# Kernel tuning notes

Hardware: AMD Instinct MI355X
Metric: run time of the kernel (lower is better)

## Reference

```python
import jax, jax.numpy as jnp
import numpy as np

N = 100000
E = 1600000
D_PCA = 50
D_BIO = 64
HID = 32
HEADS = 4
OUT = 50
EPS = 1e-5


def setup_inputs() -> dict:
    key = jax.random.key(0)
    ks = jax.random.split(key, 32)
    g = lambda i, shape, s=0.05: jax.random.normal(ks[i], shape, dtype=jnp.float32) * s
    inp = {
        'x_pca': jax.random.normal(ks[0], (N, D_PCA), dtype=jnp.float32),
        'x_bio': jax.random.normal(ks[1], (N, D_BIO), dtype=jnp.float32),
        'edge_index': jax.random.randint(ks[2], (2, E), 0, N, dtype=jnp.int32),
        # bio encoder: Linear(64,16) -> BN(16) -> ELU -> Linear(16,16) -> ELU
        'bioW1': g(3, (16, D_BIO)), 'biob1': g(4, (16,)),
        'bn0_g': 1.0 + g(5, (16,)), 'bn0_b': g(6, (16,)),
        'bn0_m': g(7, (16,)), 'bn0_v': 1.0 + 0.1 * jax.random.uniform(ks[8], (16,), dtype=jnp.float32),
        'bioW2': g(9, (16, 16)), 'biob2': g(10, (16,)),
        # GATv2 layer 1: in = 50+16 = 66, out = HEADS*HID concat
        'Wl1': g(11, (HEADS * HID, D_PCA + 16)), 'bl1': g(12, (HEADS * HID,)),
        'Wr1': g(13, (HEADS * HID, D_PCA + 16)), 'br1': g(14, (HEADS * HID,)),
        'att1': g(15, (HEADS, HID)), 'bias1': g(16, (HEADS * HID,)),
        'bn1_g': 1.0 + g(17, (HEADS * HID,)), 'bn1_b': g(18, (HEADS * HID,)),
        'bn1_m': g(19, (HEADS * HID,)), 'bn1_v': 1.0 + 0.1 * jax.random.uniform(ks[20], (HEADS * HID,), dtype=jnp.float32),
        # GATv2 layer 2: in = HEADS*HID, heads=1, concat=False
        'Wl2': g(21, (HID, HEADS * HID)), 'bl2': g(22, (HID,)),
        'Wr2': g(23, (HID, HEADS * HID)), 'br2': g(24, (HID,)),
        'att2': g(25, (1, HID)), 'bias2': g(26, (HID,)),
        'bn2_g': 1.0 + g(27, (HID,)), 'bn2_b': g(28, (HID,)),
        'bn2_m': g(29, (HID,)), 'bn2_v': 1.0 + 0.1 * jax.random.uniform(ks[30], (HID,), dtype=jnp.float32),
        'predW': g(31, (OUT, HID)), 'predb': jnp.zeros((OUT,), dtype=jnp.float32),
    }
    return inp


def _bn(h, gm, bt, mean, var):
    # BatchNorm1d in eval mode (running stats)
    return (h - mean) * jax.lax.rsqrt(var + EPS) * gm + bt


def _gatv2(x, src, dst, Wl, bl, Wr, br, att, bias, heads, out_dim, concat):
    n = x.shape[0]
    xl = (x @ Wl.T + bl).reshape(n, heads, out_dim)  # source transform
    xr = (x @ Wr.T + br).reshape(n, heads, out_dim)  # target transform
    e = jax.nn.leaky_relu(xl[src] + xr[dst], 0.2)    # [E,H,C]
    logits = jnp.einsum('ehc,hc->eh', e, att)        # [E,H]
    m = jax.ops.segment_max(logits, dst, num_segments=n)
    a = jnp.exp(logits - m[dst])
    denom = jax.ops.segment_sum(a, dst, num_segments=n)
    alpha = a / (denom[dst] + 1e-16)                 # segment softmax over dst
    out = jax.ops.segment_sum(xl[src] * alpha[..., None], dst, num_segments=n)
    out = out.reshape(n, heads * out_dim) if concat else out.mean(axis=1)
    return out + bias


def reference(x_pca, x_bio, edge_index,
              bioW1, biob1, bn0_g, bn0_b, bn0_m, bn0_v, bioW2, biob2,
              Wl1, bl1, Wr1, br1, att1, bias1, bn1_g, bn1_b, bn1_m, bn1_v,
              Wl2, bl2, Wr2, br2, att2, bias2, bn2_g, bn2_b, bn2_m, bn2_v,
              predW, predb):
    n = x_pca.shape[0]
    # add self-loops (PyG GATv2Conv default)
    loop = jnp.arange(n, dtype=edge_index.dtype)
    src = jnp.concatenate([edge_index[0], loop])
    dst = jnp.concatenate([edge_index[1], loop])

    # bio encoder
    h_bio = jax.nn.elu(_bn(x_bio @ bioW1.T + biob1, bn0_g, bn0_b, bn0_m, bn0_v))
    h_bio = jax.nn.elu(h_bio @ bioW2.T + biob2)
    x = jnp.concatenate([x_pca, h_bio], axis=1)  # [N, 66]

    h = _gatv2(x, src, dst, Wl1, bl1, Wr1, br1, att1, bias1, HEADS, HID, True)
    h = jax.nn.elu(_bn(h, bn1_g, bn1_b, bn1_m, bn1_v))  # dropout off (eval)
    h = _gatv2(h, src, dst, Wl2, bl2, Wr2, br2, att2, bias2, 1, HID, False)
    h = jax.nn.elu(_bn(h, bn2_g, bn2_b, bn2_m, bn2_v))
    return h @ predW.T + predb
```

## Files before the change

kernel.cpp:

```cpp
#include <hip/hip_runtime.h>
#include <hip/hip_fp16.h>
#include <cstdint>
#include <cstddef>

#define NN 100000
#define NE 1600000
#define NEP (NE + NN)
#define NBLK 200
#define CHUNK ((NEP + NBLK - 1) / NBLK)
#define NBUCK2 ((NN + 255) / 256)
#define HISTN (NBUCK2 * NBLK)
#define HSCAN_BLOCKS ((HISTN + 1023) / 1024)

typedef __attribute__((ext_vector_type(8))) _Float16 half8;
typedef __attribute__((ext_vector_type(4))) _Float16 h4v;
typedef __attribute__((ext_vector_type(2))) _Float16 h2v;
typedef __attribute__((ext_vector_type(4))) float float4v;

__device__ __forceinline__ float elu_f(float x) {
    return x > 0.f ? x : __expf(x) - 1.f;
}

__device__ __forceinline__ float ex2(float x) {
#if __has_builtin(__builtin_amdgcn_exp2f)
    return __builtin_amdgcn_exp2f(x);
#else
    return exp2f(x);
#endif
}

template<int CTRL>
__device__ __forceinline__ float dpp_add(float x) {
    int s = __builtin_amdgcn_update_dpp(0, __float_as_int(x), CTRL, 0xF, 0xF, true);
    return x + __int_as_float(s);
}
__device__ __forceinline__ float sum4_all(float x) {
    x = dpp_add<0xB1>(x); x = dpp_add<0x4E>(x);
    return x;
}
__device__ __forceinline__ float sum8_all(float x) {
    x = dpp_add<0xB1>(x); x = dpp_add<0x4E>(x); x = dpp_add<0x141>(x);
    return x;
}

__device__ __forceinline__ float dot2f(h2v a, h2v b, float c) {
#if __has_builtin(__builtin_amdgcn_fdot2)
    return __builtin_amdgcn_fdot2(a, b, c, false);
#else
    return fmaf((float)a[0], (float)b[0], fmaf((float)a[1], (float)b[1], c));
#endif
}

__device__ __forceinline__ h2v hmax2v(h2v a, h2v b) {
#if __has_builtin(__builtin_elementwise_max)
    return __builtin_elementwise_max(a, b);
#else
    __half2 r = __hmax2(*(__half2*)&a, *(__half2*)&b);
    return *(h2v*)&r;
#endif
}


__global__ __launch_bounds__(256) void part_hist(const int* __restrict__ ei, int* __restrict__ hist)
{
    __shared__ int cnt[NBUCK2];
    int tid = threadIdx.x, k = blockIdx.x;
    for (int i = tid; i < NBUCK2; i += 256) cnt[i] = 0;
    __syncthreads();
    int e0 = k * CHUNK, e1 = min(e0 + CHUNK, NEP);
    for (int e = e0 + tid; e < e1; e += 256) {
        int dst = (e < NE) ? ei[NE + e] : e - NE;
        atomicAdd(&cnt[dst >> 8], 1);
    }
    __syncthreads();
    for (int i = tid; i < NBUCK2; i += 256) hist[i * NBLK + k] = cnt[i];
}

__global__ __launch_bounds__(256) void scan_p1(const int* __restrict__ src, int* __restrict__ part, int n)
{
    __shared__ int wsum[4];
    int t = threadIdx.x;
    int i0 = blockIdx.x * 1024 + t * 4;
    int s = 0;
    if (i0 + 3 < n) { int4 d = *(const int4*)(src + i0); s = d.x + d.y + d.z + d.w; }
    else { for (int k = 0; k < 4; k++) if (i0 + k < n) s += src[i0 + k]; }
    for (int d = 1; d < 64; d <<= 1) s += __shfl_xor(s, d, 64);
    if ((t & 63) == 0) wsum[t >> 6] = s;
    __syncthreads();
    if (t == 0) part[blockIdx.x] = wsum[0] + wsum[1] + wsum[2] + wsum[3];
}

__global__ __launch_bounds__(128) void scan_p2(int* __restrict__ part, int nb, int* __restrict__ off)
{
    __shared__ int wt[2];
    int t = threadIdx.x;
    int lane = t & 63, w = t >> 6;
    int v = (t < nb) ? part[t] : 0;
    int x = v;
    for (int d = 1; d < 64; d <<= 1) { int y = __shfl_up(x, d, 64); if (lane >= d) x += y; }
    if (lane == 63) wt[w] = x;
    __syncthreads();
    int base = (w == 1) ? wt[0] : 0;
    int excl = base + x - v;
    if (t < nb) part[t] = excl;
    if (t == 0) off[NN] = NEP;
}

__global__ __launch_bounds__(256) void scan_p3(int* __restrict__ data, const int* __restrict__ part, int n)
{
    __shared__ int wsum[4];
    int t = threadIdx.x, lane = t & 63, w = t >> 6;
    int i0 = blockIdx.x * 1024 + t * 4;
    int d0 = 0, d1 = 0, d2 = 0, d3 = 0;
    if (i0 + 3 < n) { int4 d = *(const int4*)(data + i0); d0 = d.x; d1 = d.y; d2 = d.z; d3 = d.w; }
    else if (i0 < n) {
        d0 = data[i0];
        if (i0 + 1 < n) d1 = data[i0 + 1];
        if (i0 + 2 < n) d2 = data[i0 + 2];
    }
    int s = d0 + d1 + d2 + d3;
    int x = s;
    for (int d = 1; d < 64; d <<= 1) { int y = __shfl_up(x, d, 64); if (lane >= d) x += y; }
    if (lane == 63) wsum[w] = x;
    __syncthreads();
    int wb = 0;
    for (int i = 0; i < w; i++) wb += wsum[i];
    int base = part[blockIdx.x] + wb + x - s;
    if (i0 < n)     data[i0]     = base;
    if (i0 + 1 < n) data[i0 + 1] = base + d0;
    if (i0 + 2 < n) data[i0 + 2] = base + d0 + d1;
    if (i0 + 3 < n) data[i0 + 3] = base + d0 + d1 + d2;
}

__global__ __launch_bounds__(256) void part_scatter(const int* __restrict__ ei,
                                                    const int* __restrict__ hist,
                                                    unsigned* __restrict__ ebuf)
{
    __shared__ int cur[NBUCK2];
    int tid = threadIdx.x, k = blockIdx.x;
    for (int i = tid; i < NBUCK2; i += 256) cur[i] = hist[i * NBLK + k];
    __syncthreads();
    int e0 = k * CHUNK, e1 = min(e0 + CHUNK, NEP);
    for (int e = e0 + tid; e < e1; e += 256) {
        int src, dst;
        if (e < NE) { src = ei[e]; dst = ei[NE + e]; } else { src = dst = e - NE; }
        int pos = atomicAdd(&cur[dst >> 8], 1);
        ebuf[pos] = (unsigned)src | ((unsigned)(dst & 255) << 24);
    }
}

__global__ __launch_bounds__(256) void bucket_csr(const int* __restrict__ hist,
                                                  const unsigned* __restrict__ ebuf,
                                                  int* __restrict__ off, int* __restrict__ csr)
{
    __shared__ int cnt[256];
    __shared__ int cur[256];
    __shared__ int wsum[4];
    int b = blockIdx.x;
    int d0 = b << 8;
    int tid = threadIdx.x;
    int e0 = hist[b * NBLK];
    int e1 = (b + 1 < NBUCK2) ? hist[(b + 1) * NBLK] : NEP;
    cnt[tid] = 0;
    __syncthreads();
    for (int i = e0 + tid; i < e1; i += 256) atomicAdd(&cnt[ebuf[i] >> 24], 1);
    __syncthreads();
    int c = cnt[tid];
    int x = c;
    int lane = tid & 63, w = tid >> 6;
    for (int d = 1; d < 64; d <<= 1) { int y = __shfl_up(x, d, 64); if (lane >= d) x += y; }
    if (lane == 63) wsum[w] = x;
    __syncthreads();
    int wb = 0;
    for (int i = 0; i < w; i++) wb += wsum[i];
    int excl = wb + x - c;
    cur[tid] = e0 + excl;
    int node = d0 + tid;
    if (node < NN) off[node] = e0 + excl;
    __syncthreads();
    for (int i = e0 + tid; i < e1; i += 256) {
        unsigned v = ebuf[i];
        int p = atomicAdd(&cur[v >> 24], 1);
        csr[p] = (int)(v & 0xFFFFFF);
    }
}


__global__ __launch_bounds__(256) void bio_kernel(
    const float* __restrict__ xb, const float* __restrict__ xp,
    const float* __restrict__ W1, const float* __restrict__ b1,
    const float* __restrict__ g0, const float* __restrict__ bb0,
    const float* __restrict__ m0, const float* __restrict__ v0,
    const float* __restrict__ W2, const float* __restrict__ b2,
    __half* __restrict__ xh)
{
    __shared__ float sW1[16*64], sW2[16*16], sb1[16], sb2[16], ss[16], st[16];
    int tid = threadIdx.x;
    for (int idx = tid; idx < 1024; idx += 256) sW1[idx] = W1[idx];
    if (tid < 256) sW2[tid] = W2[tid];
    if (tid < 16) {
        sb1[tid] = b1[tid]; sb2[tid] = b2[tid];
        float s = g0[tid] * rsqrtf(v0[tid] + 1e-5f);
        ss[tid] = s; st[tid] = bb0[tid] - m0[tid] * s;
    }
    __syncthreads();
    int i = blockIdx.x * 256 + tid;
    if (i >= NN) return;
    float bio[64];
    const float4* p = (const float4*)(xb + (size_t)i * 64);
    #pragma unroll
    for (int q = 0; q < 16; q++) {
        float4 f = p[q];
        bio[q*4] = f.x; bio[q*4+1] = f.y; bio[q*4+2] = f.z; bio[q*4+3] = f.w;
    }
    float t1[16];
    #pragma unroll
    for (int j = 0; j < 16; j++) {
        float acc = sb1[j];
        #pragma unroll
        for (int k = 0; k < 64; k++) acc += bio[k] * sW1[j*64 + k];
        acc = acc * ss[j] + st[j];
        t1[j] = elu_f(acc);
    }
    __half* xrow = xh + (size_t)i * 96;
    const float* xpr = xp + (size_t)i * 50;
    #pragma unroll
    for (int j = 0; j < 25; j++) {
        float2 f = *(const float2*)(xpr + 2 * j);
        *(__half2*)(xrow + 2 * j) = __floats2half2_rn(f.x, f.y);
    }
    #pragma unroll
    for (int j = 0; j < 16; j++) {
        float acc = sb2[j];
        #pragma unroll
        for (int k = 0; k < 16; k++) acc += t1[k] * sW2[j*16 + k];
        xrow[50 + j] = __float2half(elu_f(acc));
    }
    __half2 z2 = __floats2half2_rn(0.f, 0.f);
    #pragma unroll
    for (int j = 0; j < 15; j++) *(__half2*)(xrow + 66 + 2 * j) = z2;
}


__global__ __launch_bounds__(256) void wconvert_all(
    const float* __restrict__ Wl1, const float* __restrict__ Wr1,
    const float* __restrict__ bl1, const float* __restrict__ br1,
    const float* __restrict__ Wl2, const float* __restrict__ Wr2,
    const float* __restrict__ bl2, const float* __restrict__ br2,
    const float* __restrict__ predW, const float* __restrict__ predb,
    const float* __restrict__ bias1, const float* __restrict__ bn1g,
    const float* __restrict__ bn1b, const float* __restrict__ bn1m,
    const float* __restrict__ bn1v,
    const float* __restrict__ bias2, const float* __restrict__ bn2g,
    const float* __restrict__ bn2b, const float* __restrict__ bn2m,
    const float* __restrict__ bn2v,
    __half* __restrict__ wcat1, float* __restrict__ bcat1,
    __half* __restrict__ wcat2, float* __restrict__ bcat2,
    __half* __restrict__ wpred, float* __restrict__ bpred,
    float* __restrict__ scb1, float* __restrict__ shb1,
    float* __restrict__ scb2, float* __restrict__ shb2)
{
    int t = blockIdx.x * 256 + threadIdx.x;
    if (t < 256 * 96) {
        int j = t / 96, k = t - j * 96;
        float v = (k < 66) ? ((j < 128) ? Wl1[j * 66 + k] : Wr1[(j - 128) * 66 + k]) : 0.f;
        wcat1[t] = __float2half(v);
    }
    int u = t - 256 * 96;
    if (u >= 0 && u < 64 * 128) {
        int j = u >> 7, k = u & 127;
        float v = (j < 32) ? Wl2[j * 128 + k] : Wr2[(j - 32) * 128 + k];
        wcat2[u] = __float2half(v);
    }
    int w = u - 64 * 128;
    if (w >= 0 && w < 64 * 32) {
        int j = w >> 5;
        wpred[w] = __float2half(j < 50 ? predW[w] : 0.f);
    }
    int z = w - 64 * 32;
    if (z >= 0 && z < 256) bcat1[z] = (z < 128) ? bl1[z] : br1[z - 128];
    int z2 = z - 256;
    if (z2 >= 0 && z2 < 64) bcat2[z2] = (z2 < 32) ? bl2[z2] : br2[z2 - 32];
    int z3 = z2 - 64;
    if (z3 >= 0 && z3 < 64) bpred[z3] = (z3 < 50) ? predb[z3] : 0.f;
    int z4 = z3 - 64;
    if (z4 >= 0 && z4 < 128) {
        float sc = bn1g[z4] * rsqrtf(bn1v[z4] + 1e-5f);
        scb1[z4] = sc;
        shb1[z4] = bn1b[z4] + (bias1[z4] - bn1m[z4]) * sc;
    }
    int z5 = z4 - 128;
    if (z5 >= 0 && z5 < 32) {
        float sc = bn2g[z5] * rsqrtf(bn2v[z5] + 1e-5f);
        scb2[z5] = sc;
        shb2[z5] = bn2b[z5] + (bias2[z5] - bn2m[z5]) * sc;
    }
}

template<int KT, int NC, bool FOUT>
__global__ __launch_bounds__(256) void mfma_gemm(
    const __half* __restrict__ in, const __half* __restrict__ wcat,
    const float* __restrict__ bcat, void* __restrict__ outv, int n, int ncol)
{
    constexpr int K = KT * 32;
    constexpr int KP = K + 8;
    __shared__ __half sW[NC * KP];
    __shared__ __half sX[64 * KP];
    __shared__ float sB[NC];
    int tid = threadIdx.x;
    for (int idx = tid * 8; idx < NC * K; idx += 256 * 8) {
        int r = idx / K, c = idx - r * K;
        *(half8*)(&sW[r * KP + c]) = *(const half8*)(&wcat[r * K + c]);
    }
    for (int idx = tid; idx < NC; idx += 256) sB[idx] = bcat[idx];
    int row0 = blockIdx.x * 64;
    half8 hz = {0, 0, 0, 0, 0, 0, 0, 0};
    for (int idx = tid * 8; idx < 64 * K; idx += 256 * 8) {
        int r = idx / K, c = idx - r * K;
        int gr = row0 + r;
        half8 v = (gr < n) ? *(const half8*)(&in[(size_t)gr * K + c]) : hz;
        *(half8*)(&sX[r * KP + c]) = v;
    }
    __syncthreads();
    int w = tid >> 6, lane = tid & 63;
    int m = lane & 15, quad = lane >> 4;
    half8 a[KT];
    #pragma unroll
    for (int kt = 0; kt < KT; kt++)
        a[kt] = *(const half8*)(&sX[(w * 16 + m) * KP + kt * 32 + quad * 8]);
    #pragma unroll 1
    for (int nt = 0; nt < NC / 16; nt++) {
        float4v acc = {0.f, 0.f, 0.f, 0.f};
        #pragma unroll
        for (int kt = 0; kt < KT; kt++) {
            half8 bfrag = *(const half8*)(&sW[(nt * 16 + m) * KP + kt * 32 + quad * 8]);
            acc = __builtin_amdgcn_mfma_f32_16x16x32_f16(a[kt], bfrag, acc, 0, 0, 0);
        }
        int col = nt * 16 + m;
        float bias = sB[col];
        #pragma unroll
        for (int i = 0; i < 4; i++) {
            int r = row0 + w * 16 + quad * 4 + i;
            if (r < n) {
                if (FOUT) { if (col < ncol) ((float*)outv)[(size_t)r * ncol + col] = acc[i] + bias; }
                else ((__half*)outv)[(size_t)r * NC + col] = __float2half(acc[i] + bias);
            }
        }
    }
}

__global__ __launch_bounds__(256) void fused_gat1(
    const int* __restrict__ off, const int* __restrict__ csr,
    const __half* __restrict__ xcat, const float* __restrict__ att,
    const float* __restrict__ scb, const float* __restrict__ shb,
    __half* __restrict__ h1)
{
    int wave = threadIdx.x >> 6;
    int lane = threadIdx.x & 63;
    int node = blockIdx.x * 4 + wave;
    if (node >= NN) return;
    int row = lane >> 4;
    int cl  = lane & 15;
    int ch  = cl * 8;
    unsigned chb = (unsigned)cl * 16u;
    const char* xbase = (const char*)xcat;
    const float LOG2E = 1.44269504088896f;

    half8 xr8 = *(const half8*)(xbase + (size_t)node * 512 + 256 + chb);
    float4 af0 = *(const float4*)(att + ch);
    float4 af1 = *(const float4*)(att + ch + 4);
    h2v a01 = {(_Float16)(af0.x * LOG2E), (_Float16)(af0.y * LOG2E)};
    h2v a23 = {(_Float16)(af0.z * LOG2E), (_Float16)(af0.w * LOG2E)};
    h2v a45 = {(_Float16)(af1.x * LOG2E), (_Float16)(af1.y * LOG2E)};
    h2v a67 = {(_Float16)(af1.z * LOG2E), (_Float16)(af1.w * LOG2E)};
    h2v xr01 = {xr8[0], xr8[1]}, xr23 = {xr8[2], xr8[3]};
    h2v xr45 = {xr8[4], xr8[5]}, xr67 = {xr8[6], xr8[7]};
    const h2v c2 = {(_Float16)0.2f, (_Float16)0.2f};

    int k0 = off[node], k1 = off[node + 1];
    float acc0 = 0.f, acc1 = 0.f, acc2 = 0.f, acc3 = 0.f;
    float acc4 = 0.f, acc5 = 0.f, acc6 = 0.f, acc7 = 0.f, denom = 0.f;

    int rowp4 = row + 4;

    auto edge = [&](half8 cur, bool valid) {
        h2v xl01 = {cur[0], cur[1]}, xl23 = {cur[2], cur[3]};
        h2v xl45 = {cur[4], cur[5]}, xl67 = {cur[6], cur[7]};
        h2v s01 = xl01 + xr01, s23 = xl23 + xr23;
        h2v s45 = xl45 + xr45, s67 = xl67 + xr67;
        h2v l01 = hmax2v(s01, s01 * c2);
        h2v l23 = hmax2v(s23, s23 * c2);
        h2v l45 = hmax2v(s45, s45 * c2);
        h2v l67 = hmax2v(s67, s67 * c2);
        float pp = dot2f(l01, a01, dot2f(l23, a23, dot2f(l45, a45, dot2f(l67, a67, 0.f))));
        pp = sum4_all(pp);
        float wgt = valid ? ex2(pp) : 0.f;
        denom += wgt;
        acc0 = fmaf((float)cur[0], wgt, acc0);
        acc1 = fmaf((float)cur[1], wgt, acc1);
        acc2 = fmaf((float)cur[2], wgt, acc2);
        acc3 = fmaf((float)cur[3], wgt, acc3);
        acc4 = fmaf((float)cur[4], wgt, acc4);
        acc5 = fmaf((float)cur[5], wgt, acc5);
        acc6 = fmaf((float)cur[6], wgt, acc6);
        acc7 = fmaf((float)cur[7], wgt, acc7);
    };

    for (int base = k0; base < k1; base += 64) {
        int nb = min(64, k1 - base);
        int mysrc = (lane < nb) ? csr[base + lane] : 0;
        int pairs = (nb + 7) >> 3;

        auto loadpair = [&](half8& A, half8& B, int j) {
            int i0 = __shfl(mysrc, j * 8 + row, 64);
            int i1 = __shfl(mysrc, j * 8 + rowp4, 64);
            A = *(const half8*)(xbase + (((unsigned)i0 << 9) + chb));
            B = *(const half8*)(xbase + (((unsigned)i1 << 9) + chb));
        };
        auto edgepair = [&](half8 A, half8 B, int j) {
            edge(A, (j * 8 + row) < nb);
            edge(B, (j * 8 + rowp4) < nb);
        };

        half8 A0, B0, A1, B1, A2, B2;
        loadpair(A0, B0, 0);
        if (pairs > 1) loadpair(A1, B1, 1);
        if (pairs > 2) loadpair(A2, B2, 2);
        int j = 0;
        while (true) {
            edgepair(A0, B0, j); if (j + 3 < pairs) loadpair(A0, B0, j + 3); if (++j >= pairs) break;
            edgepair(A1, B1, j); if (j + 3 < pairs) loadpair(A1, B1, j + 3); if (++j >= pairs) break;
            edgepair(A2, B2, j); if (j + 3 < pairs) loadpair(A2, B2, j + 3); if (++j >= pairs) break;
        }
    }
    acc0 += __shfl_xor(acc0, 16, 64); acc0 += __shfl_xor(acc0, 32, 64);
    acc1 += __shfl_xor(acc1, 16, 64); acc1 += __shfl_xor(acc1, 32, 64);
    acc2 += __shfl_xor(acc2, 16, 64); acc2 += __shfl_xor(acc2, 32, 64);
    acc3 += __shfl_xor(acc3, 16, 64); acc3 += __shfl_xor(acc3, 32, 64);
    acc4 += __shfl_xor(acc4, 16, 64); acc4 += __shfl_xor(acc4, 32, 64);
    acc5 += __shfl_xor(acc5, 16, 64); acc5 += __shfl_xor(acc5, 32, 64);
    acc6 += __shfl_xor(acc6, 16, 64); acc6 += __shfl_xor(acc6, 32, 64);
    acc7 += __shfl_xor(acc7, 16, 64); acc7 += __shfl_xor(acc7, 32, 64);
    denom += __shfl_xor(denom, 16, 64); denom += __shfl_xor(denom, 32, 64);
    if (row == 0) {
        float inv = 1.f / (denom + 1e-16f);
        float4 s0 = *(const float4*)(scb + ch), s1 = *(const float4*)(scb + ch + 4);
        float4 h0 = *(const float4*)(shb + ch), h1f = *(const float4*)(shb + ch + 4);
        float o[8];
        o[0] = elu_f(fmaf(acc0 * inv, s0.x, h0.x));
        o[1] = elu_f(fmaf(acc1 * inv, s0.y, h0.y));
        o[2] = elu_f(fmaf(acc2 * inv, s0.z, h0.z));
        o[3] = elu_f(fmaf(acc3 * inv, s0.w, h0.w));
        o[4] = elu_f(fmaf(acc4 * inv, s1.x, h1f.x));
        o[5] = elu_f(fmaf(acc5 * inv, s1.y, h1f.y));
        o[6] = elu_f(fmaf(acc6 * inv, s1.z, h1f.z));
        o[7] = elu_f(fmaf(acc7 * inv, s1.w, h1f.w));
        half8 oh = {(_Float16)o[0], (_Float16)o[1], (_Float16)o[2], (_Float16)o[3],
                    (_Float16)o[4], (_Float16)o[5], (_Float16)o[6], (_Float16)o[7]};
        *(half8*)(h1 + (size_t)node * 128 + ch) = oh;
    }
}

__global__ __launch_bounds__(256) void fused_gat2(
    const int* __restrict__ off, const int* __restrict__ csr,
    const __half* __restrict__ xcat2, const float* __restrict__ att,
    const float* __restrict__ scb, const float* __restrict__ shb,
    __half* __restrict__ h2)
{
    int wave = threadIdx.x >> 6;
    int lane = threadIdx.x & 63;
    int node = blockIdx.x * 4 + wave;
    if (node >= NN) return;
    int row = lane >> 3;
    int cl  = lane & 7;
    int ch  = cl * 4;
    unsigned chb = (unsigned)cl * 8u;
    const char* xbase = (const char*)xcat2;
    const float LOG2E = 1.44269504088896f;

    h4v xr4 = *(const h4v*)(xbase + (size_t)node * 128 + 64 + chb);
    h2v xr01 = {xr4[0], xr4[1]}, xr23 = {xr4[2], xr4[3]};
    float4 af = *(const float4*)(att + ch);
    h2v a01 = {(_Float16)(af.x * LOG2E), (_Float16)(af.y * LOG2E)};
    h2v a23 = {(_Float16)(af.z * LOG2E), (_Float16)(af.w * LOG2E)};
    const h2v c2 = {(_Float16)0.2f, (_Float16)0.2f};

    int k0 = off[node], k1 = off[node + 1];
    float acc0 = 0.f, acc1 = 0.f, acc2 = 0.f, acc3 = 0.f, denom = 0.f;

    int rowp8 = row + 8;

    auto edge = [&](h4v cur, bool valid) {
        h2v xl01 = {cur[0], cur[1]}, xl23 = {cur[2], cur[3]};
        h2v s01 = xl01 + xr01, s23 = xl23 + xr23;
        h2v l01 = hmax2v(s01, s01 * c2);
        h2v l23 = hmax2v(s23, s23 * c2);
        float pp = dot2f(l01, a01, dot2f(l23, a23, 0.f));
        pp = sum8_all(pp);
        float wgt = valid ? ex2(pp) : 0.f;
        denom += wgt;
        acc0 = fmaf((float)cur[0], wgt, acc0);
        acc1 = fmaf((float)cur[1], wgt, acc1);
        acc2 = fmaf((float)cur[2], wgt, acc2);
        acc3 = fmaf((float)cur[3], wgt, acc3);
    };

    for (int base = k0; base < k1; base += 64) {
        int nb = min(64, k1 - base);
        int mysrc = (lane < nb) ? csr[base + lane] : 0;
        int pairs = (nb + 15) >> 4;

        auto loadpair = [&](h4v& A, h4v& B, int j) {
            int i0 = __shfl(mysrc, j * 16 + row, 64);
            int i1 = __shfl(mysrc, j * 16 + rowp8, 64);
            A = *(const h4v*)(xbase + (((unsigned)i0 << 7) + chb));
            B = *(const h4v*)(xbase + (((unsigned)i1 << 7) + chb));
        };
        auto edgepair = [&](h4v A, h4v B, int j) {
            edge(A, (j * 16 + row) < nb);
            edge(B, (j * 16 + rowp8) < nb);
        };

        h4v A0, B0, A1, B1, A2, B2;
        loadpair(A0, B0, 0);
        if (pairs > 1) loadpair(A1, B1, 1);
        if (pairs > 2) loadpair(A2, B2, 2);
        int j = 0;
        while (true) {
            edgepair(A0, B0, j); if (j + 3 < pairs) loadpair(A0, B0, j + 3); if (++j >= pairs) break;
            edgepair(A1, B1, j); if (j + 3 < pairs) loadpair(A1, B1, j + 3); if (++j >= pairs) break;
            edgepair(A2, B2, j); if (j + 3 < pairs) loadpair(A2, B2, j + 3); if (++j >= pairs) break;
        }
    }
    acc0 += __shfl_xor(acc0, 8, 64); acc0 += __shfl_xor(acc0, 16, 64); acc0 += __shfl_xor(acc0, 32, 64);
    acc1 += __shfl_xor(acc1, 8, 64); acc1 += __shfl_xor(acc1, 16, 64); acc1 += __shfl_xor(acc1, 32, 64);
    acc2 += __shfl_xor(acc2, 8, 64); acc2 += __shfl_xor(acc2, 16, 64); acc2 += __shfl_xor(acc2, 32, 64);
    acc3 += __shfl_xor(acc3, 8, 64); acc3 += __shfl_xor(acc3, 16, 64); acc3 += __shfl_xor(acc3, 32, 64);
    denom += __shfl_xor(denom, 8, 64); denom += __shfl_xor(denom, 16, 64); denom += __shfl_xor(denom, 32, 64);
    if (row == 0) {
        float inv = 1.f / (denom + 1e-16f);
        float4 sv = *(const float4*)(scb + ch);
        float4 hv = *(const float4*)(shb + ch);
        float o0 = elu_f(fmaf(acc0 * inv, sv.x, hv.x));
        float o1 = elu_f(fmaf(acc1 * inv, sv.y, hv.y));
        float o2 = elu_f(fmaf(acc2 * inv, sv.z, hv.z));
        float o3 = elu_f(fmaf(acc3 * inv, sv.w, hv.w));
        h4v oh = {(_Float16)o0, (_Float16)o1, (_Float16)o2, (_Float16)o3};
        *(h4v*)(h2 + (size_t)node * 32 + ch) = oh;
    }
}

extern "C" void kernel_launch(void* const* d_in, const int* in_sizes, int n_in,
                              void* d_out, int out_size, void* d_ws, size_t ws_size,
                              hipStream_t stream)
{
    const float* x_pca = (const float*)d_in[0];
    const float* x_bio = (const float*)d_in[1];
    const int*   ei    = (const int*)d_in[2];
    const float* bioW1 = (const float*)d_in[3];
    const float* biob1 = (const float*)d_in[4];
    const float* bn0_g = (const float*)d_in[5];
    const float* bn0_b = (const float*)d_in[6];
    const float* bn0_m = (const float*)d_in[7];
    const float* bn0_v = (const float*)d_in[8];
    const float* bioW2 = (const float*)d_in[9];
    const float* biob2 = (const float*)d_in[10];
    const float* Wl1   = (const float*)d_in[11];
    const float* bl1   = (const float*)d_in[12];
    const float* Wr1   = (const float*)d_in[13];
    const float* br1   = (const float*)d_in[14];
    const float* att1  = (const float*)d_in[15];
    const float* bias1 = (const float*)d_in[16];
    const float* bn1_g = (const float*)d_in[17];
    const float* bn1_b = (const float*)d_in[18];
    const float* bn1_m = (const float*)d_in[19];
    const float* bn1_v = (const float*)d_in[20];
    const float* Wl2   = (const float*)d_in[21];
    const float* bl2   = (const float*)d_in[22];
    const float* Wr2   = (const float*)d_in[23];
    const float* br2   = (const float*)d_in[24];
    const float* att2  = (const float*)d_in[25];
    const float* bias2 = (const float*)d_in[26];
    const float* bn2_g = (const float*)d_in[27];
    const float* bn2_b = (const float*)d_in[28];
    const float* bn2_m = (const float*)d_in[29];
    const float* bn2_v = (const float*)d_in[30];
    const float* predW = (const float*)d_in[31];
    const float* predb = (const float*)d_in[32];

    float* ws = (float*)d_ws;
    __half* xh    = (__half*)ws;
    float*  p0    = ws + 4800000;
    __half* xcat1 = (__half*)p0;
    float*  p1    = p0 + 12800000;
    __half* h1h   = (__half*)p1;
    float*  p2    = p1 + 6400000;
    __half* xcat2 = (__half*)p2;
    float*  p3    = p2 + 3200000;
    __half* h2h   = (__half*)p3;
    float*  p4    = p3 + 1600000;
    __half* wcat1 = (__half*)p4;
    float*  bcat1 = p4 + 12288;
    __half* wcat2 = (__half*)(bcat1 + 256);
    float*  bcat2 = bcat1 + 256 + 4096;
    __half* wpred = (__half*)(bcat2 + 64);
    float*  bpred = bcat2 + 64 + 1024;
    float*  scb1  = bpred + 64;
    float*  shb1  = scb1 + 128;
    float*  scb2  = shb1 + 128;
    float*  shb2  = scb2 + 32;
    int*    ib    = (int*)(shb2 + 32);
    unsigned* ebuf = (unsigned*)ib;
    int*    hist   = ib + NEP;
    int*    part   = hist + HISTN;
    int*    off    = part + 128;
    int*    csr    = off + NN + 1;

    float* out = (float*)d_out;

    part_hist<<<NBLK, 256, 0, stream>>>(ei, hist);
    scan_p1<<<HSCAN_BLOCKS, 256, 0, stream>>>(hist, part, HISTN);
    scan_p2<<<1, 128, 0, stream>>>(part, HSCAN_BLOCKS, off);
    scan_p3<<<HSCAN_BLOCKS, 256, 0, stream>>>(hist, part, HISTN);
    part_scatter<<<NBLK, 256, 0, stream>>>(ei, hist, ebuf);
    bucket_csr<<<NBUCK2, 256, 0, stream>>>(hist, ebuf, off, csr);

    bio_kernel<<<(NN + 255) / 256, 256, 0, stream>>>(
        x_bio, x_pca, bioW1, biob1, bn0_g, bn0_b, bn0_m, bn0_v, bioW2, biob2, xh);

    wconvert_all<<<139, 256, 0, stream>>>(
        Wl1, Wr1, bl1, br1, Wl2, Wr2, bl2, br2, predW, predb,
        bias1, bn1_g, bn1_b, bn1_m, bn1_v,
        bias2, bn2_g, bn2_b, bn2_m, bn2_v,
        wcat1, bcat1, wcat2, bcat2, wpred, bpred,
        scb1, shb1, scb2, shb2);

    mfma_gemm<3, 256, false><<<(NN + 63) / 64, 256, 0, stream>>>(xh, wcat1, bcat1, xcat1, NN, 0);

    fused_gat1<<<(NN + 3) / 4, 256, 0, stream>>>(
        off, csr, xcat1, att1, scb1, shb1, h1h);

    mfma_gemm<4, 64, false><<<(NN + 63) / 64, 256, 0, stream>>>(h1h, wcat2, bcat2, xcat2, NN, 0);

    fused_gat2<<<(NN + 3) / 4, 256, 0, stream>>>(
        off, csr, xcat2, att2, scb2, shb2, h2h);

    mfma_gemm<1, 64, true><<<(NN + 63) / 64, 256, 0, stream>>>(h2h, wpred, bpred, out, NN, 50);
}
```

Measured before the change: 413.2 us.

## Split GATv2 source/target projections into separate arrays and simplify gather prefetch

The GEMM now writes the source (xl) and target (xr) projections to two separate contiguous arrays instead of one interleaved row. The gather in both GAT kernels then reads from a denser xl table with half the row stride, which is meant to improve cache and TLB locality for the random source-node gathers. The triple-buffered prefetch loop is replaced by a simpler one-step-ahead prefetch that clamps the lane index, dropping prefetch depth in exchange for less register pressure and control flow. The clamped extra loads at the tail fetch redundant rows.

```diff
diff --git a/kernel.cpp b/kernel.cpp
--- a/kernel.cpp
+++ b/kernel.cpp
@@ -297,10 +297,11 @@
     }
 }
 
-template<int KT, int NC, bool FOUT>
+template<int KT, int NC, int NSPL, bool FOUT>
 __global__ __launch_bounds__(256) void mfma_gemm(
     const __half* __restrict__ in, const __half* __restrict__ wcat,
-    const float* __restrict__ bcat, void* __restrict__ outv, int n, int ncol)
+    const float* __restrict__ bcat, void* __restrict__ outv, void* __restrict__ outv2,
+    int n, int ncol)
 {
     constexpr int K = KT * 32;
     constexpr int KP = K + 8;
@@ -343,7 +344,10 @@
             int r = row0 + w * 16 + quad * 4 + i;
             if (r < n) {
                 if (FOUT) { if (col < ncol) ((float*)outv)[(size_t)r * ncol + col] = acc[i] + bias; }
-                else ((__half*)outv)[(size_t)r * NC + col] = __float2half(acc[i] + bias);
+                else if (col < NSPL)
+                    ((__half*)outv)[(size_t)r * NSPL + col] = __float2half(acc[i] + bias);
+                else
+                    ((__half*)outv2)[(size_t)r * (NC - NSPL) + (col - NSPL)] = __float2half(acc[i] + bias);
             }
         }
     }
@@ -351,7 +355,8 @@
 
 __global__ __launch_bounds__(256) void fused_gat1(
     const int* __restrict__ off, const int* __restrict__ csr,
-    const __half* __restrict__ xcat, const float* __restrict__ att,
+    const __half* __restrict__ xl, const __half* __restrict__ xr,
+    const float* __restrict__ att,
     const float* __restrict__ scb, const float* __restrict__ shb,
     __half* __restrict__ h1)
 {
@@ -363,10 +368,10 @@
     int cl  = lane & 15;
     int ch  = cl * 8;
     unsigned chb = (unsigned)cl * 16u;
-    const char* xbase = (const char*)xcat;
+    const char* xbase = (const char*)xl;
     const float LOG2E = 1.44269504088896f;
 
-    half8 xr8 = *(const half8*)(xbase + (size_t)node * 512 + 256 + chb);
+    half8 xr8 = *(const half8*)((const char*)xr + (size_t)node * 256 + chb);
     float4 af0 = *(const float4*)(att + ch);
     float4 af1 = *(const float4*)(att + ch + 4);
     h2v a01 = {(_Float16)(af0.x * LOG2E), (_Float16)(af0.y * LOG2E)};
@@ -381,7 +386,9 @@
     float acc0 = 0.f, acc1 = 0.f, acc2 = 0.f, acc3 = 0.f;
     float acc4 = 0.f, acc5 = 0.f, acc6 = 0.f, acc7 = 0.f, denom = 0.f;
 
-    int rowp4 = row + 4;
+    int rowp4  = row + 4;
+    int rowp8  = row + 8;
+    int rowp12 = row + 12;
 
     auto edge = [&](half8 cur, bool valid) {
         h2v xl01 = {cur[0], cur[1]}, xl23 = {cur[2], cur[3]};
@@ -409,28 +416,19 @@
     for (int base = k0; base < k1; base += 64) {
         int nb = min(64, k1 - base);
         int mysrc = (lane < nb) ? csr[base + lane] : 0;
-        int pairs = (nb + 7) >> 3;
-
-        auto loadpair = [&](half8& A, half8& B, int j) {
-            int i0 = __shfl(mysrc, j * 8 + row, 64);
-            int i1 = __shfl(mysrc, j * 8 + rowp4, 64);
-            A = *(const half8*)(xbase + (((unsigned)i0 << 9) + chb));
-            B = *(const half8*)(xbase + (((unsigned)i1 << 9) + chb));
-        };
-        auto edgepair = [&](half8 A, half8 B, int j) {
-            edge(A, (j * 8 + row) < nb);
-            edge(B, (j * 8 + rowp4) < nb);
-        };
-
-        half8 A0, B0, A1, B1, A2, B2;
-        loadpair(A0, B0, 0);
-        if (pairs > 1) loadpair(A1, B1, 1);
-        if (pairs > 2) loadpair(A2, B2, 2);
-        int j = 0;
-        while (true) {
-            edgepair(A0, B0, j); if (j + 3 < pairs) loadpair(A0, B0, j + 3); if (++j >= pairs) break;
-            edgepair(A1, B1, j); if (j + 3 < pairs) loadpair(A1, B1, j + 3); if (++j >= pairs) break;
-            edgepair(A2, B2, j); if (j + 3 < pairs) loadpair(A2, B2, j + 3); if (++j >= pairs) break;
+        int nbm1 = nb - 1;
+        int i0 = __shfl(mysrc, min(row, nbm1), 64);
+        int i1 = __shfl(mysrc, min(rowp4, nbm1), 64);
+        half8 c0 = *(const half8*)(xbase + (((unsigned)i0 << 8) + chb));
+        half8 c1 = *(const half8*)(xbase + (((unsigned)i1 << 8) + chb));
+        for (int t = 0; t < nb; t += 8) {
+            int i2 = __shfl(mysrc, min(t + rowp8, nbm1), 64);
+            int i3 = __shfl(mysrc, min(t + rowp12, nbm1), 64);
+            half8 cc2 = *(const half8*)(xbase + (((unsigned)i2 << 8) + chb));
+            half8 cc3 = *(const half8*)(xbase + (((unsigned)i3 << 8) + chb));
+            edge(c0, (t + row) < nb);
+            edge(c1, (t + rowp4) < nb);
+            c0 = cc2; c1 = cc3;
         }
     }
     acc0 += __shfl_xor(acc0, 16, 64); acc0 += __shfl_xor(acc0, 32, 64);
@@ -463,7 +461,8 @@
 
 __global__ __launch_bounds__(256) void fused_gat2(
     const int* __restrict__ off, const int* __restrict__ csr,
-    const __half* __restrict__ xcat2, const float* __restrict__ att,
+    const __half* __restrict__ xl2, const __half* __restrict__ xr2,
+    const float* __restrict__ att,
     const float* __restrict__ scb, const float* __restrict__ shb,
     __half* __restrict__ h2)
 {
@@ -475,10 +474,10 @@
     int cl  = lane & 7;
     int ch  = cl * 4;
     unsigned chb = (unsigned)cl * 8u;
-    const char* xbase = (const char*)xcat2;
+    const char* xbase = (const char*)xl2;
     const float LOG2E = 1.44269504088896f;
 
-    h4v xr4 = *(const h4v*)(xbase + (size_t)node * 128 + 64 + chb);
+    h4v xr4 = *(const h4v*)((const char*)xr2 + (size_t)node * 64 + chb);
     h2v xr01 = {xr4[0], xr4[1]}, xr23 = {xr4[2], xr4[3]};
     float4 af = *(const float4*)(att + ch);
     h2v a01 = {(_Float16)(af.x * LOG2E), (_Float16)(af.y * LOG2E)};
@@ -488,7 +487,9 @@
     int k0 = off[node], k1 = off[node + 1];
     float acc0 = 0.f, acc1 = 0.f, acc2 = 0.f, acc3 = 0.f, denom = 0.f;
 
-    int rowp8 = row + 8;
+    int rowp8  = row + 8;
+    int rowp16 = row + 16;
+    int rowp24 = row + 24;
 
     auto edge = [&](h4v cur, bool valid) {
         h2v xl01 = {cur[0], cur[1]}, xl23 = {cur[2], cur[3]};
@@ -508,28 +509,19 @@
     for (int base = k0; base < k1; base += 64) {
         int nb = min(64, k1 - base);
         int mysrc = (lane < nb) ? csr[base + lane] : 0;
-        int pairs = (nb + 15) >> 4;
-
-        auto loadpair = [&](h4v& A, h4v& B, int j) {
-            int i0 = __shfl(mysrc, j * 16 + row, 64);
-            int i1 = __shfl(mysrc, j * 16 + rowp8, 64);
-            A = *(const h4v*)(xbase + (((unsigned)i0 << 7) + chb));
-            B = *(const h4v*)(xbase + (((unsigned)i1 << 7) + chb));
-        };
-        auto edgepair = [&](h4v A, h4v B, int j) {
-            edge(A, (j * 16 + row) < nb);
-            edge(B, (j * 16 + rowp8) < nb);
-        };
-
-        h4v A0, B0, A1, B1, A2, B2;
-        loadpair(A0, B0, 0);
-        if (pairs > 1) loadpair(A1, B1, 1);
-        if (pairs > 2) loadpair(A2, B2, 2);
-        int j = 0;
-        while (true) {
-            edgepair(A0, B0, j); if (j + 3 < pairs) loadpair(A0, B0, j + 3); if (++j >= pairs) break;
-            edgepair(A1, B1, j); if (j + 3 < pairs) loadpair(A1, B1, j + 3); if (++j >= pairs) break;
-            edgepair(A2, B2, j); if (j + 3 < pairs) loadpair(A2, B2, j + 3); if (++j >= pairs) break;
+        int nbm1 = nb - 1;
+        int i0 = __shfl(mysrc, min(row, nbm1), 64);
+        int i1 = __shfl(mysrc, min(rowp8, nbm1), 64);
+        h4v c0 = *(const h4v*)(xbase + (((unsigned)i0 << 6) + chb));
+        h4v c1 = *(const h4v*)(xbase + (((unsigned)i1 << 6) + chb));
+        for (int t = 0; t < nb; t += 16) {
+            int i2 = __shfl(mysrc, min(t + rowp16, nbm1), 64);
+            int i3 = __shfl(mysrc, min(t + rowp24, nbm1), 64);
+            h4v cc2 = *(const h4v*)(xbase + (((unsigned)i2 << 6) + chb));
+            h4v cc3 = *(const h4v*)(xbase + (((unsigned)i3 << 6) + chb));
+            edge(c0, (t + row) < nb);
+            edge(c1, (t + rowp8) < nb);
+            c0 = cc2; c1 = cc3;
         }
     }
     acc0 += __shfl_xor(acc0, 8, 64); acc0 += __shfl_xor(acc0, 16, 64); acc0 += __shfl_xor(acc0, 32, 64);
@@ -588,17 +580,14 @@
     const float* predW = (const float*)d_in[31];
     const float* predb = (const float*)d_in[32];
 
-    float* ws = (float*)d_ws;
-    __half* xh    = (__half*)ws;
-    float*  p0    = ws + 4800000;
-    __half* xcat1 = (__half*)p0;
-    float*  p1    = p0 + 12800000;
-    __half* h1h   = (__half*)p1;
-    float*  p2    = p1 + 6400000;
-    __half* xcat2 = (__half*)p2;
-    float*  p3    = p2 + 3200000;
-    __half* h2h   = (__half*)p3;
-    float*  p4    = p3 + 1600000;
+    __half* xh   = (__half*)d_ws;
+    __half* xl1  = xh  + (size_t)NN * 96;
+    __half* xr1  = xl1 + (size_t)NN * 128;
+    __half* h1h  = xr1 + (size_t)NN * 128;
+    __half* xl2  = h1h + (size_t)NN * 128;
+    __half* xr2  = xl2 + (size_t)NN * 32;
+    __half* h2h  = xr2 + (size_t)NN * 32;
+    float*  p4   = (float*)(h2h + (size_t)NN * 32);
     __half* wcat1 = (__half*)p4;
     float*  bcat1 = p4 + 12288;
     __half* wcat2 = (__half*)(bcat1 + 256);
@@ -635,15 +624,18 @@
         wcat1, bcat1, wcat2, bcat2, wpred, bpred,
         scb1, shb1, scb2, shb2);
 
-    mfma_gemm<3, 256, false><<<(NN + 63) / 64, 256, 0, stream>>>(xh, wcat1, bcat1, xcat1, NN, 0);
+    mfma_gemm<3, 256, 128, false><<<(NN + 63) / 64, 256, 0, stream>>>(
+        xh, wcat1, bcat1, xl1, xr1, NN, 0);
 
     fused_gat1<<<(NN + 3) / 4, 256, 0, stream>>>(
-        off, csr, xcat1, att1, scb1, shb1, h1h);
-
-    mfma_gemm<4, 64, false><<<(NN + 63) / 64, 256, 0, stream>>>(h1h, wcat2, bcat2, xcat2, NN, 0);
+        off, csr, xl1, xr1, att1, scb1, shb1, h1h);
+
+    mfma_gemm<4, 64, 32, false><<<(NN + 63) / 64, 256, 0, stream>>>(
+        h1h, wcat2, bcat2, xl2, xr2, NN, 0);
 
     fused_gat2<<<(NN + 3) / 4, 256, 0, stream>>>(
-        off, csr, xcat2, att2, scb2, shb2, h2h);
-
-    mfma_gemm<1, 64, true><<<(NN + 63) / 64, 256, 0, stream>>>(h2h, wpred, bpred, out, NN, 50);
-}
+        off, csr, xl2, xr2, att2, scb2, shb2, h2h);
+
+    mfma_gemm<1, 64, 64, true><<<(NN + 63) / 64, 256, 0, stream>>>(
+        h2h, wpred, bpred, out, nullptr, NN, 50);
+}
```

Result: faster. 399.4 us (-3.4%).
